# Kernel tuning notes

Measured on AMD Instinct MI355X. Metric: run time of the kernel, lower is better.

Reference implementation:

```python
import jax, jax.numpy as jnp
import numpy as np

D_MODEL = 1024
D_HID = D_MODEL // 4
N_EXPERTS = 64
TOP_K = 2


def setup_inputs() -> dict:
    key = jax.random.key(0)
    k_x, k_w1, k_b1, k_w2, k_b2 = jax.random.split(key, 5)
    # torch Linear default init: U(-1/sqrt(fan_in), 1/sqrt(fan_in))
    s1 = 1.0 / np.sqrt(D_MODEL)
    s2 = 1.0 / np.sqrt(D_HID)
    return {
        "x": jax.random.normal(k_x, (4, 4096, D_MODEL), dtype=jnp.float32),
        "W1": jax.random.uniform(k_w1, (D_MODEL, D_HID), jnp.float32, -s1, s1),
        "b1": jax.random.uniform(k_b1, (D_HID,), jnp.float32, -s1, s1),
        "W2": jax.random.uniform(k_w2, (D_HID, N_EXPERTS), jnp.float32, -s2, s2),
        "b2": jax.random.uniform(k_b2, (N_EXPERTS,), jnp.float32, -s2, s2),
    }


def reference(x, W1, b1, W2, b2):
    # gate MLP: [B,S,D] -> [B,S,H] -> tanh -> [B,S,E]
    h = jnp.tanh(jnp.einsum("bsd,dh->bsh", x, W1) + b1)
    gate_logits = jnp.einsum("bsh,he->bse", h, W2) + b2
    # top-k selection + softmax over the k selected logits
    top_logits, top_idx = jax.lax.top_k(gate_logits, TOP_K)  # [B,S,K]
    top_gates = jax.nn.softmax(top_logits, axis=-1)          # [B,S,K]
    # scatter back into dense [B,S,E] gate tensor
    onehot = jax.nn.one_hot(top_idx, N_EXPERTS, dtype=top_gates.dtype)  # [B,S,K,E]
    gates = jnp.einsum("bsk,bske->bse", top_gates, onehot)
    return gates, gate_logits
```

## Files before the change

### kernel.cpp

```cpp
#include <hip/hip_runtime.h>
#include <math.h>


#define DM 1024
#define DH 256
#define NE 64
#define BM 64
#define BN 128
#define BK 32

#define W1P_OFF 0
#define W1P_STRIDE 524288
#define W2P_OFF 1572864
#define W2P_STRIDE 32768
#define H_OFF 1671168

typedef __attribute__((ext_vector_type(8))) short bf16x8;
typedef __attribute__((ext_vector_type(4))) float f32x4;

__device__ __forceinline__ unsigned fbits(float f) { return __float_as_uint(f); }
__device__ __forceinline__ float topf(unsigned u) { return __uint_as_float(u & 0xFFFF0000u); }

__device__ __forceinline__ void split3(float v, unsigned& h, unsigned& m, unsigned& l) {
    h = fbits(v);
    float r1 = v - topf(h);
    m = fbits(r1);
    float r2 = r1 - topf(m);
    l = fbits(r2);
}
__device__ __forceinline__ unsigned packpair(unsigned a, unsigned b) {
    return (a >> 16) | (b & 0xFFFF0000u);
}
__device__ __forceinline__ bf16x8 as_bf(uint4 u) {
    union { uint4 a; bf16x8 b; } c; c.a = u; return c.b;
}


__global__ __launch_bounds__(256)
void prep_planes(const float* __restrict__ W1, const float* __restrict__ W2,
                 char* __restrict__ ws) {
    unsigned* w1p = (unsigned*)(ws + W1P_OFF);
    unsigned* w2p = (unsigned*)(ws + W2P_OFF);
    const int gt = blockIdx.x * 256 + threadIdx.x;
    if (gt < 131072) {
        const int q = gt & 3, L = (gt >> 2) & 63, nt = (gt >> 8) & 15, kc = gt >> 12;
        const int n = nt * 16 + (L & 15);
        const int k0 = kc * 32 + ((L >> 4) & 3) * 8 + 2 * q;
        float v0 = W1[(size_t)k0 * DH + n];
        float v1 = W1[(size_t)(k0 + 1) * DH + n];
        unsigned h0, m0, l0, h1, m1, l1;
        split3(v0, h0, m0, l0);
        split3(v1, h1, m1, l1);
        w1p[0 * 131072 + gt] = packpair(h0, h1);
        w1p[1 * 131072 + gt] = packpair(m0, m1);
        w1p[2 * 131072 + gt] = packpair(l0, l1);
    } else {
        const int g2 = gt - 131072;
        if (g2 < 8192) {
            const int q = g2 & 3, L = (g2 >> 2) & 63, nt = (g2 >> 8) & 3, kc = g2 >> 10;
            const int n = nt * 16 + (L & 15);
            const int k0 = kc * 32 + ((L >> 4) & 3) * 8 + 2 * q;
            float v0 = W2[k0 * NE + n];
            float v1 = W2[(k0 + 1) * NE + n];
            unsigned h0, m0, l0, h1, m1, l1;
            split3(v0, h0, m0, l0);
            split3(v1, h1, m1, l1);
            w2p[0 * 8192 + g2] = packpair(h0, h1);
            w2p[1 * 8192 + g2] = packpair(m0, m1);
            w2p[2 * 8192 + g2] = packpair(l0, l1);
        }
    }
}

__device__ __forceinline__ void cvt_store(float4 a, float4 b, char* wb) {
    float v[8] = {a.x, a.y, a.z, a.w, b.x, b.y, b.z, b.w};
    unsigned hh[8], mm[8], ll[8];
#pragma unroll
    for (int j = 0; j < 8; j++) split3(v[j], hh[j], mm[j], ll[j]);
    uint4 dh = {packpair(hh[0], hh[1]), packpair(hh[2], hh[3]),
                packpair(hh[4], hh[5]), packpair(hh[6], hh[7])};
    uint4 dm = {packpair(mm[0], mm[1]), packpair(mm[2], mm[3]),
                packpair(mm[4], mm[5]), packpair(mm[6], mm[7])};
    uint4 dl = {packpair(ll[0], ll[1]), packpair(ll[2], ll[3]),
                packpair(ll[4], ll[5]), packpair(ll[6], ll[7])};
    *(uint4*)(wb + 0)    = dh;
    *(uint4*)(wb + 4096) = dm;
    *(uint4*)(wb + 8192) = dl;
}

__global__ __launch_bounds__(256, 2)
void gemm1_mfma(const float* __restrict__ x, const char* __restrict__ w1p,
                const float* __restrict__ b1, float* __restrict__ h) {
    __shared__ __align__(16) char lds[2][12288];

    const int tid  = threadIdx.x;
    const int lane = tid & 63;
    const int wave = tid >> 6;
    const int t0 = blockIdx.x * BM;
    const int n0 = blockIdx.y * BN;

    const int stok = tid >> 2;
    const int slr  = tid & 3;
    const int sms  = stok >> 4;
    const int sL   = slr * 16 + (stok & 15);
    char* wb0 = &lds[0][sms * 1024 + sL * 16];
    char* wb1 = &lds[1][sms * 1024 + sL * 16];
    const float* xg = x + (size_t)(t0 + stok) * DM + slr * 8;

    const char* btile = w1p + (size_t)(blockIdx.y * 8 + wave * 2) * 1024 + lane * 16;

    f32x4 acc[4][2];
#pragma unroll
    for (int i = 0; i < 4; i++)
#pragma unroll
        for (int j = 0; j < 2; j++) acc[i][j] = (f32x4){0.f, 0.f, 0.f, 0.f};

    {
        float4 xa = *(const float4*)(xg);
        float4 xb = *(const float4*)(xg + 4);
        cvt_store(xa, xb, wb0);
    }
    uint4 bc[3][2];
#pragma unroll
    for (int p = 0; p < 3; p++)
#pragma unroll
        for (int nt = 0; nt < 2; nt++)
            bc[p][nt] = *(const uint4*)(btile + p * W1P_STRIDE + nt * 1024);
    __syncthreads();

    for (int kc = 0; kc < 32; kc++) {
        const bool pre = (kc + 1) < 32;
        float4 xna, xnb;
        uint4 bn[3][2];
        if (pre) {
            xna = *(const float4*)(xg + (kc + 1) * 32);
            xnb = *(const float4*)(xg + (kc + 1) * 32 + 4);
#pragma unroll
            for (int p = 0; p < 3; p++)
#pragma unroll
                for (int nt = 0; nt < 2; nt++)
                    bn[p][nt] = *(const uint4*)(btile + p * W1P_STRIDE + (kc + 1) * 16384 + nt * 1024);
        }

        const char* abase = &lds[kc & 1][lane * 16];
        bf16x8 af[3][4];
#pragma unroll
        for (int p = 0; p < 3; p++)
#pragma unroll
            for (int ms = 0; ms < 4; ms++)
                af[p][ms] = *(const bf16x8*)(abase + (p * 4 + ms) * 1024);

#pragma unroll
        for (int ms = 0; ms < 4; ms++)
#pragma unroll
            for (int nt = 0; nt < 2; nt++) {
                f32x4 a = acc[ms][nt];
                a = __builtin_amdgcn_mfma_f32_16x16x32_bf16(af[0][ms], as_bf(bc[0][nt]), a, 0, 0, 0);
                a = __builtin_amdgcn_mfma_f32_16x16x32_bf16(af[0][ms], as_bf(bc[1][nt]), a, 0, 0, 0);
                a = __builtin_amdgcn_mfma_f32_16x16x32_bf16(af[1][ms], as_bf(bc[0][nt]), a, 0, 0, 0);
                a = __builtin_amdgcn_mfma_f32_16x16x32_bf16(af[0][ms], as_bf(bc[2][nt]), a, 0, 0, 0);
                a = __builtin_amdgcn_mfma_f32_16x16x32_bf16(af[2][ms], as_bf(bc[0][nt]), a, 0, 0, 0);
                a = __builtin_amdgcn_mfma_f32_16x16x32_bf16(af[1][ms], as_bf(bc[1][nt]), a, 0, 0, 0);
                acc[ms][nt] = a;
            }

        if (pre) {
            cvt_store(xna, xnb, (kc & 1) ? wb0 : wb1);
#pragma unroll
            for (int p = 0; p < 3; p++)
#pragma unroll
                for (int nt = 0; nt < 2; nt++) bc[p][nt] = bn[p][nt];
        }
        __syncthreads();
    }

    const int rq = lane >> 4;
    const int l15 = lane & 15;
#pragma unroll
    for (int nt = 0; nt < 2; nt++) {
        const int hid = n0 + (wave * 2 + nt) * 16 + l15;
        const float bias = b1[hid];
#pragma unroll
        for (int ms = 0; ms < 4; ms++) {
            const int tokb = t0 + ms * 16 + rq * 4;
#pragma unroll
            for (int r = 0; r < 4; r++)
                h[(size_t)(tokb + r) * DH + hid] = tanhf(acc[ms][nt][r] + bias);
        }
    }
}

__global__ __launch_bounds__(256)
void gate_kernel(const float* __restrict__ h, const char* __restrict__ w2p,
                 const float* __restrict__ b2, float* __restrict__ gates,
                 float* __restrict__ logits_out) {
    const int tid = threadIdx.x;
    const int lane = tid & 63;
    const int wave = tid >> 6;
    const int l15 = lane & 15;
    const int lq = lane >> 4;
    const int tok16 = blockIdx.x * 64 + wave * 16;

    const float* hb = h + (size_t)(tok16 + l15) * DH + lq * 8;
    const char* bt = w2p + lane * 16;

    f32x4 acc[4];
#pragma unroll
    for (int nt = 0; nt < 4; nt++) acc[nt] = (f32x4){0.f, 0.f, 0.f, 0.f};

    for (int kc = 0; kc < 8; kc++) {
        float4 f0 = *(const float4*)(hb + kc * 32);
        float4 f1 = *(const float4*)(hb + kc * 32 + 4);
        float v[8] = {f0.x, f0.y, f0.z, f0.w, f1.x, f1.y, f1.z, f1.w};
        unsigned hh[8], mm[8], ll[8];
#pragma unroll
        for (int j = 0; j < 8; j++) split3(v[j], hh[j], mm[j], ll[j]);
        uint4 ah = {packpair(hh[0], hh[1]), packpair(hh[2], hh[3]),
                    packpair(hh[4], hh[5]), packpair(hh[6], hh[7])};
        uint4 am = {packpair(mm[0], mm[1]), packpair(mm[2], mm[3]),
                    packpair(mm[4], mm[5]), packpair(mm[6], mm[7])};
        uint4 al = {packpair(ll[0], ll[1]), packpair(ll[2], ll[3]),
                    packpair(ll[4], ll[5]), packpair(ll[6], ll[7])};
        bf16x8 afh = as_bf(ah), afm = as_bf(am), afl = as_bf(al);
#pragma unroll
        for (int nt = 0; nt < 4; nt++) {
            const char* tb = bt + (kc * 4 + nt) * 1024;
            bf16x8 bh = *(const bf16x8*)(tb + 0 * W2P_STRIDE);
            bf16x8 bm = *(const bf16x8*)(tb + 1 * W2P_STRIDE);
            bf16x8 bl = *(const bf16x8*)(tb + 2 * W2P_STRIDE);
            f32x4 a = acc[nt];
            a = __builtin_amdgcn_mfma_f32_16x16x32_bf16(afh, bh, a, 0, 0, 0);
            a = __builtin_amdgcn_mfma_f32_16x16x32_bf16(afh, bm, a, 0, 0, 0);
            a = __builtin_amdgcn_mfma_f32_16x16x32_bf16(afm, bh, a, 0, 0, 0);
            a = __builtin_amdgcn_mfma_f32_16x16x32_bf16(afh, bl, a, 0, 0, 0);
            a = __builtin_amdgcn_mfma_f32_16x16x32_bf16(afl, bh, a, 0, 0, 0);
            a = __builtin_amdgcn_mfma_f32_16x16x32_bf16(afm, bm, a, 0, 0, 0);
            acc[nt] = a;
        }
    }

    float b2v[4];
#pragma unroll
    for (int nt = 0; nt < 4; nt++) b2v[nt] = b2[nt * 16 + l15];

#pragma unroll
    for (int r = 0; r < 4; r++) {
        float v[4]; int e[4];
#pragma unroll
        for (int nt = 0; nt < 4; nt++) { v[nt] = acc[nt][r] + b2v[nt]; e[nt] = nt * 16 + l15; }

        float a1 = v[0], a2 = v[1]; int j1 = e[0], j2 = e[1];
        if (v[1] > v[0]) { a1 = v[1]; j1 = e[1]; a2 = v[0]; j2 = e[0]; }
#pragma unroll
        for (int t = 2; t < 4; t++) {
            if (v[t] > a1) { a2 = a1; j2 = j1; a1 = v[t]; j1 = e[t]; }
            else if (v[t] > a2) { a2 = v[t]; j2 = e[t]; }
        }
#pragma unroll
        for (int off = 1; off < 16; off <<= 1) {
            float ob1 = __shfl_xor(a1, off, 64); int oj1 = __shfl_xor(j1, off, 64);
            float ob2 = __shfl_xor(a2, off, 64); int oj2 = __shfl_xor(j2, off, 64);
            bool bw = (ob1 > a1) || (ob1 == a1 && oj1 < j1);
            float w1v = bw ? ob1 : a1; int w1i = bw ? oj1 : j1;
            float lv = bw ? a1 : ob1;  int li  = bw ? j1 : oj1;
            float rv = bw ? ob2 : a2;  int ri  = bw ? oj2 : j2;
            bool cw = (lv > rv) || (lv == rv && li < ri);
            a1 = w1v; j1 = w1i;
            a2 = cw ? lv : rv; j2 = cw ? li : ri;
        }
        float ex = __expf(a2 - a1);
        float inv = 1.f / (1.f + ex);
        float g1 = inv, g2 = ex * inv;

        const size_t row = (size_t)(tok16 + lq * 4 + r) * NE;
#pragma unroll
        for (int nt = 0; nt < 4; nt++) {
            float gv = (e[nt] == j1) ? g1 : ((e[nt] == j2) ? g2 : 0.f);
            gates[row + e[nt]] = gv;
            logits_out[row + e[nt]] = v[nt];
        }
    }
}

extern "C" void kernel_launch(void* const* d_in, const int* in_sizes, int n_in,
                              void* d_out, int out_size, void* d_ws, size_t ws_size,
                              hipStream_t stream) {
    const float* x  = (const float*)d_in[0];
    const float* W1 = (const float*)d_in[1];
    const float* b1 = (const float*)d_in[2];
    const float* W2 = (const float*)d_in[3];
    const float* b2 = (const float*)d_in[4];

    const int T = in_sizes[0] / DM;
    char* ws = (char*)d_ws;
    float* hbuf = (float*)(ws + H_OFF);
    float* gates  = (float*)d_out;
    float* logits = (float*)d_out + (size_t)T * NE;

    prep_planes<<<(131072 + 8192) / 256, 256, 0, stream>>>(W1, W2, ws);
    gemm1_mfma<<<dim3(T / BM, 2), 256, 0, stream>>>(x, ws + W1P_OFF, b1, hbuf);
    gate_kernel<<<T / 64, 256, 0, stream>>>(hbuf, ws + W2P_OFF, b2, gates, logits);
}
```

Measured before the change: 153.0 us.

## Fuse gate MLP GEMMs into one kernel keeping hidden activations in LDS

Merges the first GEMM (x·W1, tanh) and the gate GEMM with top-2 softmax into one 512-thread kernel per 64-token tile. The hidden tile stays in padded shared memory rather than going through a global buffer, which removes that round trip and one launch. Each wave now loads x straight from global into registers and splits it into bf16 planes in registers, dropping the LDS staging and per-iteration barriers. The cost is that x is loaded and split redundantly across the four column waves, W1 fragments are loaded without prefetch, and only half the waves do the second stage.

```diff
diff --git a/kernel.cpp b/kernel.cpp
--- a/kernel.cpp
+++ b/kernel.cpp
@@ -5,15 +5,13 @@
 #define DM 1024
 #define DH 256
 #define NE 64
-#define BM 64
-#define BN 128
-#define BK 32
 
 #define W1P_OFF 0
 #define W1P_STRIDE 524288
 #define W2P_OFF 1572864
 #define W2P_STRIDE 32768
-#define H_OFF 1671168
+
+#define HSTR 276
 
 typedef __attribute__((ext_vector_type(8))) short bf16x8;
 typedef __attribute__((ext_vector_type(4))) float f32x4;
@@ -33,6 +31,21 @@
 }
 __device__ __forceinline__ bf16x8 as_bf(uint4 u) {
     union { uint4 a; bf16x8 b; } c; c.a = u; return c.b;
+}
+
+__device__ __forceinline__ void split_pack8(float4 f0, float4 f1,
+                                            bf16x8& H, bf16x8& M, bf16x8& L) {
+    float v[8] = {f0.x, f0.y, f0.z, f0.w, f1.x, f1.y, f1.z, f1.w};
+    unsigned hb[8], mb[8], lb[8];
+#pragma unroll
+    for (int j = 0; j < 8; j++) split3(v[j], hb[j], mb[j], lb[j]);
+    uint4 uh = {packpair(hb[0], hb[1]), packpair(hb[2], hb[3]),
+                packpair(hb[4], hb[5]), packpair(hb[6], hb[7])};
+    uint4 um = {packpair(mb[0], mb[1]), packpair(mb[2], mb[3]),
+                packpair(mb[4], mb[5]), packpair(mb[6], mb[7])};
+    uint4 ul = {packpair(lb[0], lb[1]), packpair(lb[2], lb[3]),
+                packpair(lb[4], lb[5]), packpair(lb[6], lb[7])};
+    H = as_bf(uh); M = as_bf(um); L = as_bf(ul);
 }
 
 
@@ -72,212 +85,166 @@
     }
 }
 
-__device__ __forceinline__ void cvt_store(float4 a, float4 b, char* wb) {
-    float v[8] = {a.x, a.y, a.z, a.w, b.x, b.y, b.z, b.w};
-    unsigned hh[8], mm[8], ll[8];
-#pragma unroll
-    for (int j = 0; j < 8; j++) split3(v[j], hh[j], mm[j], ll[j]);
-    uint4 dh = {packpair(hh[0], hh[1]), packpair(hh[2], hh[3]),
-                packpair(hh[4], hh[5]), packpair(hh[6], hh[7])};
-    uint4 dm = {packpair(mm[0], mm[1]), packpair(mm[2], mm[3]),
-                packpair(mm[4], mm[5]), packpair(mm[6], mm[7])};
-    uint4 dl = {packpair(ll[0], ll[1]), packpair(ll[2], ll[3]),
-                packpair(ll[4], ll[5]), packpair(ll[6], ll[7])};
-    *(uint4*)(wb + 0)    = dh;
-    *(uint4*)(wb + 4096) = dm;
-    *(uint4*)(wb + 8192) = dl;
-}
-
-__global__ __launch_bounds__(256, 2)
-void gemm1_mfma(const float* __restrict__ x, const char* __restrict__ w1p,
-                const float* __restrict__ b1, float* __restrict__ h) {
-    __shared__ __align__(16) char lds[2][12288];
+__global__ __launch_bounds__(512, 2)
+void fused_gating(const float* __restrict__ x, const char* __restrict__ w1p,
+                  const float* __restrict__ b1, const char* __restrict__ w2p,
+                  const float* __restrict__ b2, float* __restrict__ gates,
+                  float* __restrict__ logits_out) {
+    __shared__ __align__(16) float hlds[64 * HSTR];
 
     const int tid  = threadIdx.x;
     const int lane = tid & 63;
     const int wave = tid >> 6;
-    const int t0 = blockIdx.x * BM;
-    const int n0 = blockIdx.y * BN;
-
-    const int stok = tid >> 2;
-    const int slr  = tid & 3;
-    const int sms  = stok >> 4;
-    const int sL   = slr * 16 + (stok & 15);
-    char* wb0 = &lds[0][sms * 1024 + sL * 16];
-    char* wb1 = &lds[1][sms * 1024 + sL * 16];
-    const float* xg = x + (size_t)(t0 + stok) * DM + slr * 8;
-
-    const char* btile = w1p + (size_t)(blockIdx.y * 8 + wave * 2) * 1024 + lane * 16;
-
-    f32x4 acc[4][2];
-#pragma unroll
-    for (int i = 0; i < 4; i++)
-#pragma unroll
-        for (int j = 0; j < 2; j++) acc[i][j] = (f32x4){0.f, 0.f, 0.f, 0.f};
-
-    {
-        float4 xa = *(const float4*)(xg);
-        float4 xb = *(const float4*)(xg + 4);
-        cvt_store(xa, xb, wb0);
-    }
-    uint4 bc[3][2];
-#pragma unroll
-    for (int p = 0; p < 3; p++)
-#pragma unroll
-        for (int nt = 0; nt < 2; nt++)
-            bc[p][nt] = *(const uint4*)(btile + p * W1P_STRIDE + nt * 1024);
+    const int wr = wave & 1;
+    const int wc = wave >> 1;
+    const int m15 = lane & 15;
+    const int lq  = lane >> 4;
+    const int t0 = blockIdx.x * 64;
+
+    const float* xr0 = x + (size_t)(t0 + wr * 32 + m15) * DM + lq * 8;
+    const float* xr1 = xr0 + (size_t)16 * DM;
+    const char* bbase = w1p + (size_t)(wc * 4) * 1024 + lane * 16;
+
+    f32x4 acc[2][4];
+#pragma unroll
+    for (int ms = 0; ms < 2; ms++)
+#pragma unroll
+        for (int nt = 0; nt < 4; nt++) acc[ms][nt] = (f32x4){0.f, 0.f, 0.f, 0.f};
+
+    float4 c00 = *(const float4*)(xr0);
+    float4 c01 = *(const float4*)(xr0 + 4);
+    float4 c10 = *(const float4*)(xr1);
+    float4 c11 = *(const float4*)(xr1 + 4);
+
+    for (int kc = 0; kc < 32; kc++) {
+        const int kn = (kc + 1) & 31;
+        float4 n00 = *(const float4*)(xr0 + kn * 32);
+        float4 n01 = *(const float4*)(xr0 + kn * 32 + 4);
+        float4 n10 = *(const float4*)(xr1 + kn * 32);
+        float4 n11 = *(const float4*)(xr1 + kn * 32 + 4);
+
+        uint4 bfr[3][4];
+#pragma unroll
+        for (int p = 0; p < 3; p++)
+#pragma unroll
+            for (int nt = 0; nt < 4; nt++)
+                bfr[p][nt] = *(const uint4*)(bbase + p * W1P_STRIDE + kc * 16384 + nt * 1024);
+
+        bf16x8 a0h, a0m, a0l, a1h, a1m, a1l;
+        split_pack8(c00, c01, a0h, a0m, a0l);
+        split_pack8(c10, c11, a1h, a1m, a1l);
+
+#pragma unroll
+        for (int nt = 0; nt < 4; nt++) {
+            const bf16x8 bh = as_bf(bfr[0][nt]);
+            const bf16x8 bm = as_bf(bfr[1][nt]);
+            const bf16x8 bl = as_bf(bfr[2][nt]);
+            f32x4 a0 = acc[0][nt];
+            a0 = __builtin_amdgcn_mfma_f32_16x16x32_bf16(a0h, bh, a0, 0, 0, 0);
+            a0 = __builtin_amdgcn_mfma_f32_16x16x32_bf16(a0h, bm, a0, 0, 0, 0);
+            a0 = __builtin_amdgcn_mfma_f32_16x16x32_bf16(a0m, bh, a0, 0, 0, 0);
+            a0 = __builtin_amdgcn_mfma_f32_16x16x32_bf16(a0h, bl, a0, 0, 0, 0);
+            a0 = __builtin_amdgcn_mfma_f32_16x16x32_bf16(a0l, bh, a0, 0, 0, 0);
+            a0 = __builtin_amdgcn_mfma_f32_16x16x32_bf16(a0m, bm, a0, 0, 0, 0);
+            acc[0][nt] = a0;
+            f32x4 a1 = acc[1][nt];
+            a1 = __builtin_amdgcn_mfma_f32_16x16x32_bf16(a1h, bh, a1, 0, 0, 0);
+            a1 = __builtin_amdgcn_mfma_f32_16x16x32_bf16(a1h, bm, a1, 0, 0, 0);
+            a1 = __builtin_amdgcn_mfma_f32_16x16x32_bf16(a1m, bh, a1, 0, 0, 0);
+            a1 = __builtin_amdgcn_mfma_f32_16x16x32_bf16(a1h, bl, a1, 0, 0, 0);
+            a1 = __builtin_amdgcn_mfma_f32_16x16x32_bf16(a1l, bh, a1, 0, 0, 0);
+            a1 = __builtin_amdgcn_mfma_f32_16x16x32_bf16(a1m, bm, a1, 0, 0, 0);
+            acc[1][nt] = a1;
+        }
+
+        c00 = n00; c01 = n01; c10 = n10; c11 = n11;
+    }
+
+#pragma unroll
+    for (int nt = 0; nt < 4; nt++) {
+        const int hid = wc * 64 + nt * 16 + m15;
+        const float bias = b1[hid];
+#pragma unroll
+        for (int ms = 0; ms < 2; ms++) {
+            const int tb = wr * 32 + ms * 16 + lq * 4;
+#pragma unroll
+            for (int r = 0; r < 4; r++)
+                hlds[(tb + r) * HSTR + hid] = tanhf(acc[ms][nt][r] + bias);
+        }
+    }
     __syncthreads();
 
-    for (int kc = 0; kc < 32; kc++) {
-        const bool pre = (kc + 1) < 32;
-        float4 xna, xnb;
-        uint4 bn[3][2];
-        if (pre) {
-            xna = *(const float4*)(xg + (kc + 1) * 32);
-            xnb = *(const float4*)(xg + (kc + 1) * 32 + 4);
-#pragma unroll
-            for (int p = 0; p < 3; p++)
-#pragma unroll
-                for (int nt = 0; nt < 2; nt++)
-                    bn[p][nt] = *(const uint4*)(btile + p * W1P_STRIDE + (kc + 1) * 16384 + nt * 1024);
-        }
-
-        const char* abase = &lds[kc & 1][lane * 16];
-        bf16x8 af[3][4];
-#pragma unroll
-        for (int p = 0; p < 3; p++)
-#pragma unroll
-            for (int ms = 0; ms < 4; ms++)
-                af[p][ms] = *(const bf16x8*)(abase + (p * 4 + ms) * 1024);
-
-#pragma unroll
-        for (int ms = 0; ms < 4; ms++)
-#pragma unroll
-            for (int nt = 0; nt < 2; nt++) {
-                f32x4 a = acc[ms][nt];
-                a = __builtin_amdgcn_mfma_f32_16x16x32_bf16(af[0][ms], as_bf(bc[0][nt]), a, 0, 0, 0);
-                a = __builtin_amdgcn_mfma_f32_16x16x32_bf16(af[0][ms], as_bf(bc[1][nt]), a, 0, 0, 0);
-                a = __builtin_amdgcn_mfma_f32_16x16x32_bf16(af[1][ms], as_bf(bc[0][nt]), a, 0, 0, 0);
-                a = __builtin_amdgcn_mfma_f32_16x16x32_bf16(af[0][ms], as_bf(bc[2][nt]), a, 0, 0, 0);
-                a = __builtin_amdgcn_mfma_f32_16x16x32_bf16(af[2][ms], as_bf(bc[0][nt]), a, 0, 0, 0);
-                a = __builtin_amdgcn_mfma_f32_16x16x32_bf16(af[1][ms], as_bf(bc[1][nt]), a, 0, 0, 0);
-                acc[ms][nt] = a;
-            }
-
-        if (pre) {
-            cvt_store(xna, xnb, (kc & 1) ? wb0 : wb1);
-#pragma unroll
-            for (int p = 0; p < 3; p++)
-#pragma unroll
-                for (int nt = 0; nt < 2; nt++) bc[p][nt] = bn[p][nt];
-        }
-        __syncthreads();
-    }
-
-    const int rq = lane >> 4;
-    const int l15 = lane & 15;
-#pragma unroll
-    for (int nt = 0; nt < 2; nt++) {
-        const int hid = n0 + (wave * 2 + nt) * 16 + l15;
-        const float bias = b1[hid];
-#pragma unroll
-        for (int ms = 0; ms < 4; ms++) {
-            const int tokb = t0 + ms * 16 + rq * 4;
-#pragma unroll
-            for (int r = 0; r < 4; r++)
-                h[(size_t)(tokb + r) * DH + hid] = tanhf(acc[ms][nt][r] + bias);
-        }
-    }
-}
-
-__global__ __launch_bounds__(256)
-void gate_kernel(const float* __restrict__ h, const char* __restrict__ w2p,
-                 const float* __restrict__ b2, float* __restrict__ gates,
-                 float* __restrict__ logits_out) {
-    const int tid = threadIdx.x;
-    const int lane = tid & 63;
-    const int wave = tid >> 6;
-    const int l15 = lane & 15;
-    const int lq = lane >> 4;
-    const int tok16 = blockIdx.x * 64 + wave * 16;
-
-    const float* hb = h + (size_t)(tok16 + l15) * DH + lq * 8;
-    const char* bt = w2p + lane * 16;
-
-    f32x4 acc[4];
-#pragma unroll
-    for (int nt = 0; nt < 4; nt++) acc[nt] = (f32x4){0.f, 0.f, 0.f, 0.f};
-
-    for (int kc = 0; kc < 8; kc++) {
-        float4 f0 = *(const float4*)(hb + kc * 32);
-        float4 f1 = *(const float4*)(hb + kc * 32 + 4);
-        float v[8] = {f0.x, f0.y, f0.z, f0.w, f1.x, f1.y, f1.z, f1.w};
-        unsigned hh[8], mm[8], ll[8];
-#pragma unroll
-        for (int j = 0; j < 8; j++) split3(v[j], hh[j], mm[j], ll[j]);
-        uint4 ah = {packpair(hh[0], hh[1]), packpair(hh[2], hh[3]),
-                    packpair(hh[4], hh[5]), packpair(hh[6], hh[7])};
-        uint4 am = {packpair(mm[0], mm[1]), packpair(mm[2], mm[3]),
-                    packpair(mm[4], mm[5]), packpair(mm[6], mm[7])};
-        uint4 al = {packpair(ll[0], ll[1]), packpair(ll[2], ll[3]),
-                    packpair(ll[4], ll[5]), packpair(ll[6], ll[7])};
-        bf16x8 afh = as_bf(ah), afm = as_bf(am), afl = as_bf(al);
-#pragma unroll
-        for (int nt = 0; nt < 4; nt++) {
-            const char* tb = bt + (kc * 4 + nt) * 1024;
-            bf16x8 bh = *(const bf16x8*)(tb + 0 * W2P_STRIDE);
-            bf16x8 bm = *(const bf16x8*)(tb + 1 * W2P_STRIDE);
-            bf16x8 bl = *(const bf16x8*)(tb + 2 * W2P_STRIDE);
-            f32x4 a = acc[nt];
-            a = __builtin_amdgcn_mfma_f32_16x16x32_bf16(afh, bh, a, 0, 0, 0);
-            a = __builtin_amdgcn_mfma_f32_16x16x32_bf16(afh, bm, a, 0, 0, 0);
-            a = __builtin_amdgcn_mfma_f32_16x16x32_bf16(afm, bh, a, 0, 0, 0);
-            a = __builtin_amdgcn_mfma_f32_16x16x32_bf16(afh, bl, a, 0, 0, 0);
-            a = __builtin_amdgcn_mfma_f32_16x16x32_bf16(afl, bh, a, 0, 0, 0);
-            a = __builtin_amdgcn_mfma_f32_16x16x32_bf16(afm, bm, a, 0, 0, 0);
-            acc[nt] = a;
-        }
-    }
-
-    float b2v[4];
-#pragma unroll
-    for (int nt = 0; nt < 4; nt++) b2v[nt] = b2[nt * 16 + l15];
-
-#pragma unroll
-    for (int r = 0; r < 4; r++) {
-        float v[4]; int e[4];
-#pragma unroll
-        for (int nt = 0; nt < 4; nt++) { v[nt] = acc[nt][r] + b2v[nt]; e[nt] = nt * 16 + l15; }
-
-        float a1 = v[0], a2 = v[1]; int j1 = e[0], j2 = e[1];
-        if (v[1] > v[0]) { a1 = v[1]; j1 = e[1]; a2 = v[0]; j2 = e[0]; }
-#pragma unroll
-        for (int t = 2; t < 4; t++) {
-            if (v[t] > a1) { a2 = a1; j2 = j1; a1 = v[t]; j1 = e[t]; }
-            else if (v[t] > a2) { a2 = v[t]; j2 = e[t]; }
-        }
-#pragma unroll
-        for (int off = 1; off < 16; off <<= 1) {
-            float ob1 = __shfl_xor(a1, off, 64); int oj1 = __shfl_xor(j1, off, 64);
-            float ob2 = __shfl_xor(a2, off, 64); int oj2 = __shfl_xor(j2, off, 64);
-            bool bw = (ob1 > a1) || (ob1 == a1 && oj1 < j1);
-            float w1v = bw ? ob1 : a1; int w1i = bw ? oj1 : j1;
-            float lv = bw ? a1 : ob1;  int li  = bw ? j1 : oj1;
-            float rv = bw ? ob2 : a2;  int ri  = bw ? oj2 : j2;
-            bool cw = (lv > rv) || (lv == rv && li < ri);
-            a1 = w1v; j1 = w1i;
-            a2 = cw ? lv : rv; j2 = cw ? li : ri;
-        }
-        float ex = __expf(a2 - a1);
-        float inv = 1.f / (1.f + ex);
-        float g1 = inv, g2 = ex * inv;
-
-        const size_t row = (size_t)(tok16 + lq * 4 + r) * NE;
-#pragma unroll
-        for (int nt = 0; nt < 4; nt++) {
-            float gv = (e[nt] == j1) ? g1 : ((e[nt] == j2) ? g2 : 0.f);
-            gates[row + e[nt]] = gv;
-            logits_out[row + e[nt]] = v[nt];
+    if (wave < 4) {
+        const float* hb = hlds + (wave * 16 + m15) * HSTR + lq * 8;
+        const char* bt = w2p + lane * 16;
+
+        f32x4 gacc[4];
+#pragma unroll
+        for (int nt = 0; nt < 4; nt++) gacc[nt] = (f32x4){0.f, 0.f, 0.f, 0.f};
+
+#pragma unroll
+        for (int kc = 0; kc < 8; kc++) {
+            float4 f0 = *(const float4*)(hb + kc * 32);
+            float4 f1 = *(const float4*)(hb + kc * 32 + 4);
+            bf16x8 afh, afm, afl;
+            split_pack8(f0, f1, afh, afm, afl);
+#pragma unroll
+            for (int nt = 0; nt < 4; nt++) {
+                const char* tb = bt + (kc * 4 + nt) * 1024;
+                bf16x8 bh = *(const bf16x8*)(tb + 0 * W2P_STRIDE);
+                bf16x8 bm = *(const bf16x8*)(tb + 1 * W2P_STRIDE);
+                bf16x8 bl = *(const bf16x8*)(tb + 2 * W2P_STRIDE);
+                f32x4 a = gacc[nt];
+                a = __builtin_amdgcn_mfma_f32_16x16x32_bf16(afh, bh, a, 0, 0, 0);
+                a = __builtin_amdgcn_mfma_f32_16x16x32_bf16(afh, bm, a, 0, 0, 0);
+                a = __builtin_amdgcn_mfma_f32_16x16x32_bf16(afm, bh, a, 0, 0, 0);
+                a = __builtin_amdgcn_mfma_f32_16x16x32_bf16(afh, bl, a, 0, 0, 0);
+                a = __builtin_amdgcn_mfma_f32_16x16x32_bf16(afl, bh, a, 0, 0, 0);
+                a = __builtin_amdgcn_mfma_f32_16x16x32_bf16(afm, bm, a, 0, 0, 0);
+                gacc[nt] = a;
+            }
+        }
+
+        float b2v[4];
+#pragma unroll
+        for (int nt = 0; nt < 4; nt++) b2v[nt] = b2[nt * 16 + m15];
+
+#pragma unroll
+        for (int r = 0; r < 4; r++) {
+            float v[4]; int e[4];
+#pragma unroll
+            for (int nt = 0; nt < 4; nt++) { v[nt] = gacc[nt][r] + b2v[nt]; e[nt] = nt * 16 + m15; }
+
+            float a1 = v[0], a2 = v[1]; int j1 = e[0], j2 = e[1];
+            if (v[1] > v[0]) { a1 = v[1]; j1 = e[1]; a2 = v[0]; j2 = e[0]; }
+#pragma unroll
+            for (int t = 2; t < 4; t++) {
+                if (v[t] > a1) { a2 = a1; j2 = j1; a1 = v[t]; j1 = e[t]; }
+                else if (v[t] > a2) { a2 = v[t]; j2 = e[t]; }
+            }
+#pragma unroll
+            for (int off = 1; off < 16; off <<= 1) {
+                float ob1 = __shfl_xor(a1, off, 64); int oj1 = __shfl_xor(j1, off, 64);
+                float ob2 = __shfl_xor(a2, off, 64); int oj2 = __shfl_xor(j2, off, 64);
+                bool bw = (ob1 > a1) || (ob1 == a1 && oj1 < j1);
+                float w1v = bw ? ob1 : a1; int w1i = bw ? oj1 : j1;
+                float lv = bw ? a1 : ob1;  int li  = bw ? j1 : oj1;
+                float rv = bw ? ob2 : a2;  int ri  = bw ? oj2 : j2;
+                bool cw = (lv > rv) || (lv == rv && li < ri);
+                a1 = w1v; j1 = w1i;
+                a2 = cw ? lv : rv; j2 = cw ? li : ri;
+            }
+            float ex = __expf(a2 - a1);
+            float inv = 1.f / (1.f + ex);
+            float g1 = inv, g2 = ex * inv;
+
+            const size_t row = (size_t)(t0 + wave * 16 + lq * 4 + r) * NE;
+#pragma unroll
+            for (int nt = 0; nt < 4; nt++) {
+                float gv = (e[nt] == j1) ? g1 : ((e[nt] == j2) ? g2 : 0.f);
+                gates[row + e[nt]] = gv;
+                logits_out[row + e[nt]] = v[nt];
+            }
         }
     }
 }
@@ -293,11 +260,10 @@
 
     const int T = in_sizes[0] / DM;
     char* ws = (char*)d_ws;
-    float* hbuf = (float*)(ws + H_OFF);
     float* gates  = (float*)d_out;
     float* logits = (float*)d_out + (size_t)T * NE;
 
     prep_planes<<<(131072 + 8192) / 256, 256, 0, stream>>>(W1, W2, ws);
-    gemm1_mfma<<<dim3(T / BM, 2), 256, 0, stream>>>(x, ws + W1P_OFF, b1, hbuf);
-    gate_kernel<<<T / 64, 256, 0, stream>>>(hbuf, ws + W2P_OFF, b2, gates, logits);
-}
+    fused_gating<<<T / 64, 512, 0, stream>>>(x, ws + W1P_OFF, b1, ws + W2P_OFF, b2,
+                                             gates, logits);
+}
```

Result: slower. 167.5 us (+9.4%).
